# Performance work log

Measured on AMD Instinct MI355X. Metric: run time of the kernel, lower is better.

Reference implementation:

```python
import jax, jax.numpy as jnp
import numpy as np

N, DIN, DOUT = 8192, 256, 128
NEG_SLOPE = 0.01         # F.leaky_relu default
MASK_VAL = -9.0e15       # from the torch source


def setup_inputs() -> dict:
    key = jax.random.key(0)
    kx, kadj, kW, kbW, ka1, ka2, kba = jax.random.split(key, 7)
    x = jax.random.normal(kx, (N, DIN), dtype=jnp.float32)
    adj = jax.random.randint(kadj, (N, N), 0, 2, dtype=jnp.int32)
    # Linear W: input_dim -> output_dim
    W = jax.random.normal(kW, (DIN, DOUT), dtype=jnp.float32) * (1.0 / np.sqrt(DIN))
    bW = jax.random.normal(kbW, (DOUT,), dtype=jnp.float32) * 0.01
    # Linear a: 2*output_dim -> 1, split into the h_i part (a1) and h_j part (a2)
    a1 = jax.random.normal(ka1, (DOUT,), dtype=jnp.float32) * (1.0 / np.sqrt(2 * DOUT))
    a2 = jax.random.normal(ka2, (DOUT,), dtype=jnp.float32) * (1.0 / np.sqrt(2 * DOUT))
    ba = jax.random.normal(kba, (), dtype=jnp.float32) * 0.01
    return {"x": x, "adj": adj, "W": W, "bW": bW, "a1": a1, "a2": a2, "ba": ba}


def reference(x, adj, W, bW, a1, a2, ba):
    # h = W x + b  -> [N, DOUT]
    h = x @ W + bW
    # e[i,j] = leaky_relu(a . [h_i, h_j] + ba) = leaky_relu(a1.h_i + a2.h_j + ba)
    s_src = h @ a1            # [N]
    s_dst = h @ a2            # [N]
    e = s_src[:, None] + s_dst[None, :] + ba   # [N, N]
    e = jnp.where(e > 0, e, NEG_SLOPE * e)
    # mask non-edges, row softmax over neighbors j
    e = jnp.where(adj > 0, e, MASK_VAL)
    alpha = jax.nn.softmax(e, axis=1)          # [N, N]
    # dropout is identity in eval mode (dropout_rate=0)
    return alpha @ h                            # [N, DOUT]
```

## Files before the change

kernel.cpp:

```cpp
#include <hip/hip_runtime.h>
#include <hip/hip_bf16.h>


#define NN 8192
#define DIN 256
#define DOUT 128
#define LOG2E 1.4426950408889634f

typedef __attribute__((ext_vector_type(8))) short short8;
typedef __attribute__((ext_vector_type(4))) float floatx4;

__global__ void prep_wt(const float* __restrict__ W, __hip_bfloat16* __restrict__ WT) {
    int e = blockIdx.x * blockDim.x + threadIdx.x;
    if (e < DIN * DOUT) {
        int k = e >> 7;
        int d = e & 127;
        WT[d * DIN + k] = __float2bfloat16(W[e]);
    }
}

__global__ __launch_bounds__(256, 4) void gat_h(
    const float* __restrict__ x, const __hip_bfloat16* __restrict__ WT,
    const float* __restrict__ bW, const float* __restrict__ a1, const float* __restrict__ a2,
    __hip_bfloat16* __restrict__ hbB, float* __restrict__ s_src, float* __restrict__ s_dst) {
    int tid = threadIdx.x;
    int w = tid >> 6, lane = tid & 63;
    int lm = lane & 15, lq = lane >> 4;
    int i0 = blockIdx.x * 32;
    int r0 = (w >> 1) * 16;
    int c0 = (w & 1) * 64;

    __shared__ float s1s[32], s2s[32];
    if (tid < 32) { s1s[tid] = 0.f; s2s[tid] = 0.f; }
    __syncthreads();

    floatx4 acc[4] = {};
#pragma unroll
    for (int kk = 0; kk < DIN; kk += 32) {
        const float4* xp = (const float4*)&x[(size_t)(i0 + r0 + lm) * DIN + kk + lq * 8];
        float4 xa = xp[0], xb = xp[1];
        union { short8 v; __hip_bfloat16 h[8]; } af;
        af.h[0] = __float2bfloat16(xa.x); af.h[1] = __float2bfloat16(xa.y);
        af.h[2] = __float2bfloat16(xa.z); af.h[3] = __float2bfloat16(xa.w);
        af.h[4] = __float2bfloat16(xb.x); af.h[5] = __float2bfloat16(xb.y);
        af.h[6] = __float2bfloat16(xb.z); af.h[7] = __float2bfloat16(xb.w);
#pragma unroll
        for (int t = 0; t < 4; t++) {
            int d = c0 + 16 * t + lm;
            short8 bf = *(const short8*)&WT[(size_t)d * DIN + kk + lq * 8];
            acc[t] = __builtin_amdgcn_mfma_f32_16x16x32_bf16(af.v, bf, acc[t], 0, 0, 0);
        }
    }
    float s1[4] = {0.f, 0.f, 0.f, 0.f}, s2[4] = {0.f, 0.f, 0.f, 0.f};
#pragma unroll
    for (int t = 0; t < 4; t++) {
        int d = c0 + 16 * t + lm;
        int f = (c0 >> 4) + t;
        float A1 = a1[d], A2 = a2[d], B = bW[d];
#pragma unroll
        for (int r = 0; r < 4; r++) {
            int k = r0 + lq * 4 + r;
            float h = acc[t][r] + B;
            hbB[(size_t)blockIdx.x * 4096 + f * 512 + (k >> 3) * 128 + lm * 8 + (k & 7)] =
                __float2bfloat16(h);
            s1[r] += h * A1;
            s2[r] += h * A2;
        }
    }
#pragma unroll
    for (int r = 0; r < 4; r++) {
        for (int m = 1; m < 16; m <<= 1) {
            s1[r] += __shfl_xor(s1[r], m, 64);
            s2[r] += __shfl_xor(s2[r], m, 64);
        }
    }
    if (lm == 0) {
#pragma unroll
        for (int r = 0; r < 4; r++) {
            int row = r0 + lq * 4 + r;
            atomicAdd(&s1s[row], s1[r]);
            atomicAdd(&s2s[row], s2[r]);
        }
    }
    __syncthreads();
    if (tid < 32) {
        s_src[i0 + tid] = s1s[tid] * LOG2E;
        s_dst[i0 + tid] = s2s[tid] * LOG2E;
    }
}

template <int NJT>
__global__ void build_mask(const int* __restrict__ adj, unsigned char* __restrict__ mask) {
    size_t gid = (size_t)blockIdx.x * blockDim.x + threadIdx.x;
    const int4* a = (const int4*)(adj + gid * 8);
    int4 v0 = a[0], v1 = a[1];
    unsigned int b = 0;
    b |= (v0.x != 0) ? 1u : 0u;
    b |= (v0.y != 0) ? 2u : 0u;
    b |= (v0.z != 0) ? 4u : 0u;
    b |= (v0.w != 0) ? 8u : 0u;
    b |= (v1.x != 0) ? 16u : 0u;
    b |= (v1.y != 0) ? 32u : 0u;
    b |= (v1.z != 0) ? 64u : 0u;
    b |= (v1.w != 0) ? 128u : 0u;
    unsigned int g = (unsigned int)gid & (NJT * 4 - 1);
    size_t pos = (gid & ~(size_t)(NJT * 4 - 1)) | ((g & 3) * NJT + (g >> 2));
    mask[pos] = (unsigned char)b;
}

__device__ inline short8 make_pfrag(unsigned int cm, float ssi, float4 cd0, float4 cd1,
                                    floatx4* accd, const short8 ones) {
    float p[8];
    float e;
    e = ssi + cd0.x; e = fmaxf(e, 0.01f * e); p[0] = (cm & 1u)   ? __builtin_amdgcn_exp2f(e) : 0.f;
    e = ssi + cd0.y; e = fmaxf(e, 0.01f * e); p[1] = (cm & 2u)   ? __builtin_amdgcn_exp2f(e) : 0.f;
    e = ssi + cd0.z; e = fmaxf(e, 0.01f * e); p[2] = (cm & 4u)   ? __builtin_amdgcn_exp2f(e) : 0.f;
    e = ssi + cd0.w; e = fmaxf(e, 0.01f * e); p[3] = (cm & 8u)   ? __builtin_amdgcn_exp2f(e) : 0.f;
    e = ssi + cd1.x; e = fmaxf(e, 0.01f * e); p[4] = (cm & 16u)  ? __builtin_amdgcn_exp2f(e) : 0.f;
    e = ssi + cd1.y; e = fmaxf(e, 0.01f * e); p[5] = (cm & 32u)  ? __builtin_amdgcn_exp2f(e) : 0.f;
    e = ssi + cd1.z; e = fmaxf(e, 0.01f * e); p[6] = (cm & 64u)  ? __builtin_amdgcn_exp2f(e) : 0.f;
    e = ssi + cd1.w; e = fmaxf(e, 0.01f * e); p[7] = (cm & 128u) ? __builtin_amdgcn_exp2f(e) : 0.f;
    union { short8 v; __hip_bfloat162 q[4]; } af;
    af.q[0] = __float22bfloat162_rn(make_float2(p[0], p[1]));
    af.q[1] = __float22bfloat162_rn(make_float2(p[2], p[3]));
    af.q[2] = __float22bfloat162_rn(make_float2(p[4], p[5]));
    af.q[3] = __float22bfloat162_rn(make_float2(p[6], p[7]));
    *accd = __builtin_amdgcn_mfma_f32_16x16x32_bf16(af.v, ones, *accd, 0, 0, 0);
    return af.v;
}

template <int NJT>
__global__ __launch_bounds__(256, 2) void gat_attn(
    const unsigned char* __restrict__ mask, const float* __restrict__ s_src,
    const float* __restrict__ s_dst, const float* __restrict__ ba_p,
    const __hip_bfloat16* __restrict__ hbB,
    float* __restrict__ num, float* __restrict__ lpart) {
    int tid = threadIdx.x;
    int w = tid >> 6, lane = tid & 63;
    int lm = lane & 15, lq = lane >> 4;
    int b = blockIdx.x;
    int ib = b & 31;
    int jh = b >> 5;
    int i0 = ib * 256 + w * 64;
    int jb0 = jh * (NJT * 32);

    union Mr { uint4 v[NJT / 16]; unsigned int u[NJT / 4]; };
    Mr mr[4];
    const unsigned char* mrow = mask + (size_t)(i0 + lm) * (NN / 8) + jh * (NJT * 4) + lq * NJT;
#pragma unroll
    for (int rg = 0; rg < 4; rg++)
#pragma unroll
        for (int q = 0; q < NJT / 16; q++)
            mr[rg].v[q] = ((const uint4*)(mrow + (size_t)rg * 16 * (NN / 8)))[q];

    float ba = ba_p[0] * LOG2E;
    float ssi[4];
#pragma unroll
    for (int rg = 0; rg < 4; rg++) ssi[rg] = s_src[i0 + rg * 16 + lm] + ba;
    const float* sd = s_dst + jb0 + lq * 8;
    const __hip_bfloat16* hb = hbB + ((size_t)(jh * NJT) * 8) * 512 + lane * 8;

    floatx4 acc[4][8] = {};
    floatx4 accd[4] = {};
    const short8 ones = { 0x3F80, 0x3F80, 0x3F80, 0x3F80, 0x3F80, 0x3F80, 0x3F80, 0x3F80 };

#pragma unroll
    for (int t = 0; t < NJT; t++) {
        float4 cd0 = *(const float4*)(sd + t * 32);
        float4 cd1 = *(const float4*)(sd + t * 32 + 4);
        short8 af[4];
#pragma unroll
        for (int rg = 0; rg < 4; rg++) {
            unsigned int cm = (mr[rg].u[t >> 2] >> ((t & 3) * 8)) & 0xFFu;
            af[rg] = make_pfrag(cm, ssi[rg], cd0, cd1, &accd[rg], ones);
        }
        const __hip_bfloat16* hbt = hb + (size_t)t * 8 * 512;
#pragma unroll
        for (int f = 0; f < 8; f++) {
            short8 bf = *(const short8*)(hbt + f * 512);
#pragma unroll
            for (int rg = 0; rg < 4; rg++)
                acc[rg][f] = __builtin_amdgcn_mfma_f32_16x16x32_bf16(af[rg], bf, acc[rg][f], 0, 0, 0);
        }
    }

    float* nb = num + ((size_t)jh * NN + i0) * DOUT;
#pragma unroll
    for (int rg = 0; rg < 4; rg++)
#pragma unroll
        for (int f = 0; f < 8; f++)
#pragma unroll
            for (int r = 0; r < 4; r++)
                __builtin_nontemporal_store(acc[rg][f][r],
                    &nb[(size_t)(rg * 16 + lq * 4 + r) * DOUT + f * 16 + lm]);
    if (lm == 0) {
#pragma unroll
        for (int rg = 0; rg < 4; rg++)
#pragma unroll
            for (int r = 0; r < 4; r++)
                lpart[(size_t)jh * NN + i0 + rg * 16 + lq * 4 + r] = accd[rg][r];
    }
}

__global__ void gat_combine(const float* __restrict__ num, const float* __restrict__ lpart,
                            float* __restrict__ out, int jsplit) {
    int gid = blockIdx.x * blockDim.x + threadIdx.x;
    int idx = gid * 4;
    int i = idx >> 7;
    float den = 0.f;
    for (int s = 0; s < jsplit; s++) den += lpart[(size_t)s * NN + i];
    float inv = 1.0f / den;
    floatx4 o = {0.f, 0.f, 0.f, 0.f};
    for (int s = 0; s < jsplit; s++) {
        floatx4 n = __builtin_nontemporal_load(
            (const floatx4*)&num[(size_t)s * NN * DOUT + idx]);
        o += n;
    }
    o *= inv;
    *(floatx4*)&out[idx] = o;
}

extern "C" void kernel_launch(void* const* d_in, const int* in_sizes, int n_in,
                              void* d_out, int out_size, void* d_ws, size_t ws_size,
                              hipStream_t stream) {
    const float* x  = (const float*)d_in[0];
    const int* adj  = (const int*)d_in[1];
    const float* W  = (const float*)d_in[2];
    const float* bW = (const float*)d_in[3];
    const float* a1 = (const float*)d_in[4];
    const float* a2 = (const float*)d_in[5];
    const float* ba = (const float*)d_in[6];
    float* out = (float*)d_out;

    char* ws = (char*)d_ws;
    __hip_bfloat16* hbB  = (__hip_bfloat16*)ws;
    __hip_bfloat16* WT   = (__hip_bfloat16*)(ws + 2097152);
    float* s_src         = (float*)(ws + 2162688);
    float* s_dst         = (float*)(ws + 2195456);
    float* lpart         = (float*)(ws + 2228224);
    unsigned char* mask  = (unsigned char*)(ws + 2752512);
    float* num           = (float*)(ws + 11141120);

    int jsplit = (ws_size >= 11141120 + (size_t)16 * NN * DOUT * 4) ? 16 : 8;

    if (jsplit == 16) build_mask<16><<<32768, 256, 0, stream>>>(adj, mask);
    else              build_mask<32><<<32768, 256, 0, stream>>>(adj, mask);
    prep_wt<<<128, 256, 0, stream>>>(W, WT);
    gat_h<<<256, 256, 0, stream>>>(x, WT, bW, a1, a2, hbB, s_src, s_dst);
    if (jsplit == 16)
        gat_attn<16><<<512, 256, 0, stream>>>(mask, s_src, s_dst, ba, hbB, num, lpart);
    else
        gat_attn<32><<<256, 256, 0, stream>>>(mask, s_src, s_dst, ba, hbB, num, lpart);
    gat_combine<<<1024, 256, 0, stream>>>(num, lpart, out, jsplit);
}
```

Baseline: 434.7 us.

## Stage h tiles into LDS with async global_load_lds triple buffering

```diff
diff --git a/kernel.cpp b/kernel.cpp
--- a/kernel.cpp
+++ b/kernel.cpp
@@ -144,6 +144,9 @@
     int i0 = ib * 256 + w * 64;
     int jb0 = jh * (NJT * 32);
 
+    __shared__ short8 bbuf[3][512];
+    __shared__ float sdl[NJT * 32];
+
     union Mr { uint4 v[NJT / 16]; unsigned int u[NJT / 4]; };
     Mr mr[4];
     const unsigned char* mrow = mask + (size_t)(i0 + lm) * (NN / 8) + jh * (NJT * 4) + lq * NJT;
@@ -157,8 +160,25 @@
     float ssi[4];
 #pragma unroll
     for (int rg = 0; rg < 4; rg++) ssi[rg] = s_src[i0 + rg * 16 + lm] + ba;
-    const float* sd = s_dst + jb0 + lq * 8;
-    const __hip_bfloat16* hb = hbB + ((size_t)(jh * NJT) * 8) * 512 + lane * 8;
+
+    const char* hb0 = (const char*)hbB + (size_t)jh * NJT * 8192;
+
+#define STAGE(tt, p)                                                                 \
+    do {                                                                             \
+        const char* g_ = hb0 + (size_t)(tt) * 8192 + tid * 16;                       \
+        char* l_ = (char*)&bbuf[p][0] + tid * 16;                                    \
+        __builtin_amdgcn_global_load_lds(                                            \
+            (const __attribute__((address_space(1))) unsigned int*)g_,               \
+            (__attribute__((address_space(3))) unsigned int*)l_, 16, 0, 0);          \
+        __builtin_amdgcn_global_load_lds(                                            \
+            (const __attribute__((address_space(1))) unsigned int*)(g_ + 4096),      \
+            (__attribute__((address_space(3))) unsigned int*)(l_ + 4096), 16, 0, 0); \
+    } while (0)
+
+    STAGE(0, 0);
+    const float* sdg = s_dst + jb0;
+    for (int k = tid; k < NJT * 32; k += 256) sdl[k] = sdg[k];
+    __syncthreads();
 
     floatx4 acc[4][8] = {};
     floatx4 accd[4] = {};
@@ -166,23 +186,32 @@
 
 #pragma unroll
     for (int t = 0; t < NJT; t++) {
-        float4 cd0 = *(const float4*)(sd + t * 32);
-        float4 cd1 = *(const float4*)(sd + t * 32 + 4);
+        if (t + 1 < NJT) {
+            STAGE(t + 1, (t + 1) % 3);
+            asm volatile("s_waitcnt vmcnt(2)" ::: "memory");
+        } else {
+            asm volatile("s_waitcnt vmcnt(0)" ::: "memory");
+        }
+        __builtin_amdgcn_s_barrier();
+        __builtin_amdgcn_sched_barrier(0);
+
+        float4 cd0 = *(const float4*)&sdl[t * 32 + lq * 8];
+        float4 cd1 = *(const float4*)&sdl[t * 32 + lq * 8 + 4];
         short8 af[4];
 #pragma unroll
         for (int rg = 0; rg < 4; rg++) {
             unsigned int cm = (mr[rg].u[t >> 2] >> ((t & 3) * 8)) & 0xFFu;
             af[rg] = make_pfrag(cm, ssi[rg], cd0, cd1, &accd[rg], ones);
         }
-        const __hip_bfloat16* hbt = hb + (size_t)t * 8 * 512;
 #pragma unroll
         for (int f = 0; f < 8; f++) {
-            short8 bf = *(const short8*)(hbt + f * 512);
+            short8 bf = bbuf[t % 3][f * 64 + lane];
 #pragma unroll
             for (int rg = 0; rg < 4; rg++)
                 acc[rg][f] = __builtin_amdgcn_mfma_f32_16x16x32_bf16(af[rg], bf, acc[rg][f], 0, 0, 0);
         }
     }
+#undef STAGE
 
     float* nb = num + ((size_t)jh * NN + i0) * DOUT;
 #pragma unroll
```

Result: no change. 431.9 us (-0.6%).
